# Performance work log

Measured on AMD Instinct MI355X. Metric: run time of the kernel, lower is better.

## Reference

```python
import jax, jax.numpy as jnp
import numpy as np

EMBED = 256
HEADS = 8
LEVELS = 4
POINTS = 4
HD = EMBED // HEADS  # 32


def _bilinear_sample(v, grid):
    """torch.F.grid_sample(mode='bilinear', padding_mode='zeros', align_corners=False).
    v: (B, C, H, W); grid: (B, Q, P, 2) with xy coords in [-1, 1].
    Returns (B, C, Q, P).
    """
    B, C, H, W = v.shape
    x = (grid[..., 0] + 1.0) * (W * 0.5) - 0.5
    y = (grid[..., 1] + 1.0) * (H * 0.5) - 0.5
    x0f = jnp.floor(x)
    y0f = jnp.floor(y)
    wx = x - x0f
    wy = y - y0f
    x0 = x0f.astype(jnp.int32)
    y0 = y0f.astype(jnp.int32)
    vf = v.reshape(B, C, H * W)

    def corner(xi, yi, w):
        valid = (xi >= 0) & (xi < W) & (yi >= 0) & (yi < H)
        idx = jnp.clip(yi, 0, H - 1) * W + jnp.clip(xi, 0, W - 1)  # (B, Q, P)
        g = jax.vmap(lambda vb, ib: jnp.take(vb, ib, axis=1))(vf, idx.reshape(B, -1))
        g = g.reshape(B, C, idx.shape[1], idx.shape[2])  # (B, C, Q, P)
        return g * (w * valid.astype(v.dtype))[:, None]

    return (corner(x0, y0, (1 - wx) * (1 - wy))
            + corner(x0 + 1, y0, wx * (1 - wy))
            + corner(x0, y0 + 1, (1 - wx) * wy)
            + corner(x0 + 1, y0 + 1, wx * wy))


def setup_inputs() -> dict:
    key = jax.random.key(0)
    ks = jax.random.split(key, 16)
    N, Q, D = 2, 8192, EMBED
    inp = {
        'query': jax.random.normal(ks[0], (N, Q, D), jnp.float32),
        'feat0': jax.random.normal(ks[1], (N, D, 64, 64), jnp.float32),
        'feat1': jax.random.normal(ks[2], (N, D, 32, 32), jnp.float32),
        'feat2': jax.random.normal(ks[3], (N, D, 16, 16), jnp.float32),
        'feat3': jax.random.normal(ks[4], (N, D, 8, 8), jnp.float32),
        'reference_points': jax.random.uniform(ks[5], (N, Q, 2), jnp.float32),
        # params stored as (in, out); equivalent math to torch Linear's x @ W.T + b
        'W_off': jax.random.normal(ks[6], (D, HEADS * LEVELS * POINTS * 2), jnp.float32) * 0.01,
        'b_off': jax.random.normal(ks[7], (HEADS * LEVELS * POINTS * 2,), jnp.float32) * 0.01,
        'W_attn': jax.random.normal(ks[8], (D, HEADS * LEVELS * POINTS), jnp.float32) * 0.02,
        'b_attn': jax.random.normal(ks[9], (HEADS * LEVELS * POINTS,), jnp.float32) * 0.02,
        'W_val': jax.random.normal(ks[10], (D, D), jnp.float32) * (1.0 / np.sqrt(D)),
        'b_val': jnp.zeros((D,), jnp.float32),
        'W_out': jax.random.normal(ks[11], (D, D), jnp.float32) * (1.0 / np.sqrt(D)),
        'b_out': jnp.zeros((D,), jnp.float32),
    }
    return inp


def reference(query, feat0, feat1, feat2, feat3, reference_points,
              W_off, b_off, W_attn, b_attn, W_val, b_val, W_out, b_out):
    feats = [feat0, feat1, feat2, feat3]
    N, Q, D = query.shape
    # offset / attention-weight projections
    off = (query @ W_off + b_off).reshape(N, Q, HEADS, LEVELS, POINTS, 2)
    attn = (query @ W_attn + b_attn).reshape(N, Q, HEADS, LEVELS, POINTS)
    # reference points (N,Q,2) -> (N,Q,L,2)
    ref = jnp.broadcast_to(reference_points[:, :, None, :], (N, Q, LEVELS, 2))
    # value projection (1x1 conv) per level, split heads -> (N*H, hd, H_l, W_l)
    vals = [(jnp.einsum('bchw,cd->bdhw', f, W_val) + b_val[None, :, None, None])
            .reshape(N * HEADS, HD, f.shape[2], f.shape[3]) for f in feats]
    # flatten batch*heads
    off = off.transpose(0, 2, 1, 3, 4, 5).reshape(N * HEADS, Q, LEVELS, POINTS, 2)
    attn = attn.transpose(0, 2, 1, 3, 4).reshape(N * HEADS, Q, LEVELS, POINTS)
    refh = jnp.broadcast_to(ref[:, None], (N, HEADS, Q, LEVELS, 2)).reshape(N * HEADS, Q, LEVELS, 2)
    loc = refh[:, :, :, None, :] + off                 # (NH, Q, L, P, 2) in [0,1]
    grid = 2.0 * loc - 1.0                             # [-1, 1]
    # per-level bilinear sampling -> (NH, hd, Q, L, P)
    sampled = jnp.stack([_bilinear_sample(vals[l], grid[:, :, l]) for l in range(LEVELS)], axis=-2)
    # softmax over levels*points
    aw = jax.nn.softmax(attn.reshape(N * HEADS, Q, LEVELS * POINTS), axis=-1)
    aw = jnp.nan_to_num(aw).reshape(N * HEADS, Q, LEVELS, POINTS)
    out = jnp.einsum('bcqlp,bqlp->bcq', sampled, aw)   # (NH, hd, Q)
    out = out.reshape(N, HEADS, HD, Q).transpose(0, 3, 1, 2).reshape(N, Q, D)
    return out @ W_out + b_out
```

## Files before the change

kernel.cpp:

```cpp
#include <hip/hip_runtime.h>
#include <math.h>

#define NB 2
#define QN 8192
#define DIM 256
#define S_TOT 5440

typedef unsigned int uint32;
typedef _Float16 f16;
typedef __attribute__((ext_vector_type(8))) _Float16 h8;
typedef __attribute__((ext_vector_type(2))) _Float16 h2;
typedef __attribute__((ext_vector_type(4))) float f32x4;
typedef __attribute__((ext_vector_type(4))) uint32 u32x4;

__global__ __launch_bounds__(256) void prep_kernel(
    const float* __restrict__ f0, const float* __restrict__ f1,
    const float* __restrict__ f2, const float* __restrict__ f3,
    const float* __restrict__ W_off, const float* __restrict__ W_attn,
    const float* __restrict__ W_val, const float* __restrict__ W_out,
    f16* __restrict__ featT, f16* __restrict__ Wcat_t,
    f16* __restrict__ Wval_t, f16* __restrict__ Wout_t) {
  const int t = blockIdx.x;
  const float* src;
  f16* dst;
  int S, tb;
  if (t < 340) {
    const int b = (t >= 170) ? 1 : 0;
    const int tt = t - 170 * b;
    int soff;
    if (tt < 128)      { src = f0; S = 4096; soff = 0;    tb = tt; }
    else if (tt < 160) { src = f1; S = 1024; soff = 4096; tb = tt - 128; }
    else if (tt < 168) { src = f2; S = 256;  soff = 5120; tb = tt - 160; }
    else               { src = f3; S = 64;   soff = 5376; tb = tt - 168; }
    src += (size_t)b * 256 * S;
    dst = featT + ((size_t)b * S_TOT + soff) * 256;
  } else {
    const int tw = t - 340;
    if (tw < 8)       { src = W_off;  dst = Wcat_t;             S = 256; tb = tw; }
    else if (tw < 12) { src = W_attn; dst = Wcat_t + 256 * 256; S = 128; tb = tw - 8; }
    else if (tw < 20) { src = W_val;  dst = Wval_t;             S = 256; tb = tw - 12; }
    else              { src = W_out;  dst = Wout_t;             S = 256; tb = tw - 20; }
  }
  const int s0 = tb * 32, c0 = blockIdx.y * 32;

  __shared__ float tile[32][33];
  const int tx = threadIdx.x & 31, ty = threadIdx.x >> 5;
#pragma unroll
  for (int j = 0; j < 4; ++j) {
    const int c = c0 + ty + j * 8;
    tile[ty + j * 8][tx] = src[(size_t)c * S + s0 + tx];
  }
  __syncthreads();
#pragma unroll
  for (int j = 0; j < 4; ++j) {
    const int srow = s0 + ty + j * 8;
    dst[(size_t)srow * 256 + c0 + tx] = (f16)tile[tx][ty + j * 8];
  }
}

__global__ __launch_bounds__(256) void gemm_fused_kernel(
    const f16* __restrict__ featT, const float* __restrict__ query,
    const f16* __restrict__ Wval_t, const f16* __restrict__ Wcat_t,
    const float* __restrict__ b_val, const float* __restrict__ b_off,
    const float* __restrict__ b_attn,
    f16* __restrict__ vals, f16* __restrict__ offb, f16* __restrict__ attnb) {
  __shared__ f16 As[64][256];
  __shared__ f16 Bs[64][256];
  const int t = blockIdx.x;
  const int tid = threadIdx.x;
  const bool isval = (t < 170);
  const size_t r0 = (size_t)(isval ? t : t - 170) * 64;
  const int NC = isval ? 4 : 6;
  const f16* Bt = isval ? Wval_t : Wcat_t;

  const int row = tid >> 5, slot = tid & 31;

#pragma unroll
  for (int i = 0; i < 8; ++i) {
    const int r = i * 8 + row;
    const int ph = (slot & 24) | ((slot ^ r) & 7);
    if (isval) {
      *(u32x4*)&As[r][ph * 8] =
          *(const u32x4*)(featT + (r0 + r) * 256 + slot * 8);
    } else {
      const float* ga = query + (r0 + r) * 256 + slot * 8;
      const float4 u0 = *(const float4*)ga;
      const float4 u1 = *(const float4*)(ga + 4);
      h8 hv = {(f16)u0.x, (f16)u0.y, (f16)u0.z, (f16)u0.w,
               (f16)u1.x, (f16)u1.y, (f16)u1.z, (f16)u1.w};
      *(h8*)&As[r][ph * 8] = hv;
    }
  }

  const int wid = tid >> 6, lane = tid & 63;
  const int wr = (wid >> 1) * 32, wc = (wid & 1) * 32;
  const int l15 = lane & 15, l4 = lane >> 4;

  u32x4 bpre[8];
#pragma unroll
  for (int i = 0; i < 8; ++i) {
    bpre[i] = *(const u32x4*)(Bt + (size_t)(i * 8 + row) * 256 + slot * 8);
  }

  h8 areg[8][2];

  for (int c = 0; c < NC; ++c) {
    __syncthreads();
#pragma unroll
    for (int i = 0; i < 8; ++i) {
      const int r = i * 8 + row;
      const int ph = (slot & 24) | ((slot ^ r) & 7);
      *(u32x4*)&Bs[r][ph * 8] = bpre[i];
    }
    __syncthreads();

    if (c + 1 < NC) {
#pragma unroll
      for (int i = 0; i < 8; ++i) {
        bpre[i] = *(const u32x4*)(Bt + (size_t)((c + 1) * 64 + i * 8 + row) * 256 + slot * 8);
      }
    }

    f32x4 acc[2][2] = {};
#pragma unroll
    for (int ks = 0; ks < 8; ++ks) {
      const int slot2 = ks * 4 + l4;
      if (c == 0) {
#pragma unroll
        for (int m = 0; m < 2; ++m) {
          const int r = wr + m * 16 + l15;
          const int ph = (slot2 & 24) | ((slot2 ^ r) & 7);
          areg[ks][m] = *(const h8*)&As[r][ph * 8];
        }
      }
      h8 b[2];
#pragma unroll
      for (int n = 0; n < 2; ++n) {
        const int r = wc + n * 16 + l15;
        const int ph = (slot2 & 24) | ((slot2 ^ r) & 7);
        b[n] = *(const h8*)&Bs[r][ph * 8];
      }
#pragma unroll
      for (int m = 0; m < 2; ++m)
#pragma unroll
        for (int n = 0; n < 2; ++n)
          acc[m][n] = __builtin_amdgcn_mfma_f32_16x16x32_f16(areg[ks][m], b[n], acc[m][n], 0, 0, 0);
    }

#pragma unroll
    for (int m = 0; m < 2; ++m)
#pragma unroll
      for (int n = 0; n < 2; ++n)
#pragma unroll
        for (int r = 0; r < 4; ++r) {
          const size_t rw = r0 + wr + m * 16 + l4 * 4 + r;
          const int col = c * 64 + wc + n * 16 + l15;
          const float v = acc[m][n][r];
          if (isval) {
            vals[rw * 256 + col] = (f16)(v + b_val[col]);
          } else if (col < 256) {
            offb[rw * 256 + col] = (f16)(v + b_off[col]);
          } else {
            attnb[rw * 128 + (col - 256)] = (f16)(v + b_attn[col - 256]);
          }
        }
  }
}

__global__ __launch_bounds__(256) void gemm_out_kernel(
    const f16* __restrict__ A, const f16* __restrict__ Bt,
    const float* __restrict__ bias, float* __restrict__ out) {
  __shared__ f16 As[64][256];
  __shared__ f16 Bs[64][256];
  const int tid = threadIdx.x;
  const size_t r0 = (size_t)blockIdx.x * 64;

  const int row = tid >> 5, slot = tid & 31;
#pragma unroll
  for (int i = 0; i < 8; ++i) {
    const int r = i * 8 + row;
    const int ph = (slot & 24) | ((slot ^ r) & 7);
    *(u32x4*)&As[r][ph * 8] = *(const u32x4*)(A + (r0 + r) * 256 + slot * 8);
  }

  const int wid = tid >> 6, lane = tid & 63;
  const int wr = (wid >> 1) * 32, wc = (wid & 1) * 32;
  const int l15 = lane & 15, l4 = lane >> 4;

  u32x4 bpre[8];
#pragma unroll
  for (int i = 0; i < 8; ++i) {
    bpre[i] = *(const u32x4*)(Bt + (size_t)(i * 8 + row) * 256 + slot * 8);
  }

  h8 areg[8][2];

  for (int c = 0; c < 4; ++c) {
    __syncthreads();
#pragma unroll
    for (int i = 0; i < 8; ++i) {
      const int r = i * 8 + row;
      const int ph = (slot & 24) | ((slot ^ r) & 7);
      *(u32x4*)&Bs[r][ph * 8] = bpre[i];
    }
    __syncthreads();

    if (c + 1 < 4) {
#pragma unroll
      for (int i = 0; i < 8; ++i) {
        bpre[i] = *(const u32x4*)(Bt + (size_t)((c + 1) * 64 + i * 8 + row) * 256 + slot * 8);
      }
    }

    f32x4 acc[2][2] = {};
#pragma unroll
    for (int ks = 0; ks < 8; ++ks) {
      const int slot2 = ks * 4 + l4;
      if (c == 0) {
#pragma unroll
        for (int m = 0; m < 2; ++m) {
          const int r = wr + m * 16 + l15;
          const int ph = (slot2 & 24) | ((slot2 ^ r) & 7);
          areg[ks][m] = *(const h8*)&As[r][ph * 8];
        }
      }
      h8 b[2];
#pragma unroll
      for (int n = 0; n < 2; ++n) {
        const int r = wc + n * 16 + l15;
        const int ph = (slot2 & 24) | ((slot2 ^ r) & 7);
        b[n] = *(const h8*)&Bs[r][ph * 8];
      }
#pragma unroll
      for (int m = 0; m < 2; ++m)
#pragma unroll
        for (int n = 0; n < 2; ++n)
          acc[m][n] = __builtin_amdgcn_mfma_f32_16x16x32_f16(areg[ks][m], b[n], acc[m][n], 0, 0, 0);
    }

#pragma unroll
    for (int m = 0; m < 2; ++m)
#pragma unroll
      for (int n = 0; n < 2; ++n)
#pragma unroll
        for (int r = 0; r < 4; ++r) {
          const size_t rw = r0 + wr + m * 16 + l4 * 4 + r;
          const int col = c * 64 + wc + n * 16 + l15;
          out[rw * 256 + col] = acc[m][n][r] + bias[col];
        }
  }
}

__global__ __launch_bounds__(256) void sample_kernel(
    const f16* __restrict__ vals, const f16* __restrict__ offb,
    const f16* __restrict__ attnb, const float* __restrict__ refp,
    f16* __restrict__ samp) {
  const int tid = threadIdx.x;
  const int g = tid & 15;
  const int grp = tid >> 4;
  const int h = grp & 7;
  const int half = tid >> 7;
  const int bq = blockIdx.x * 2 + half;
  const int b = bq >> 13;

  __shared__ float4 wts[16][17];
  __shared__ int4 idxs[16][17];

  const float rx = refp[(size_t)bq * 2 + 0];
  const float ry = refp[(size_t)bq * 2 + 1];

  float logit = (float)attnb[(size_t)bq * 128 + h * 16 + g];
  float m = logit;
#pragma unroll
  for (int mask = 1; mask < 16; mask <<= 1)
    m = fmaxf(m, __shfl_xor(m, mask, 16));
  const float e = __expf(logit - m);
  float ssum = e;
#pragma unroll
  for (int mask = 1; mask < 16; mask <<= 1)
    ssum += __shfl_xor(ssum, mask, 16);
  const float aw = e / ssum;

  const h2 ov = *(const h2*)(offb + (size_t)bq * 256 + h * 32 + g * 2);
  const int l = g >> 2;
  const int Wl = 64 >> l;
  const int loff = (l == 0) ? 0 : (l == 1) ? 4096 : (l == 2) ? 5120 : 5376;

  const float px = (rx + (float)ov[0]) * (float)Wl - 0.5f;
  const float py = (ry + (float)ov[1]) * (float)Wl - 0.5f;
  const float fx = floorf(px), fy = floorf(py);
  const float wx = px - fx, wy = py - fy;
  const int x0 = (int)fx, y0 = (int)fy;
  const int x1 = x0 + 1, y1 = y0 + 1;
  const float vx0 = (x0 >= 0 && x0 < Wl) ? 1.f : 0.f;
  const float vx1 = (x1 >= 0 && x1 < Wl) ? 1.f : 0.f;
  const float vy0 = (y0 >= 0 && y0 < Wl) ? 1.f : 0.f;
  const float vy1 = (y1 >= 0 && y1 < Wl) ? 1.f : 0.f;
  const int cx0 = min(max(x0, 0), Wl - 1), cx1 = min(max(x1, 0), Wl - 1);
  const int cy0 = min(max(y0, 0), Wl - 1), cy1 = min(max(y1, 0), Wl - 1);
  const int base = b * S_TOT + loff;
  idxs[grp][g] = make_int4((base + cy0 * Wl + cx0) * 512,
                           (base + cy0 * Wl + cx1) * 512,
                           (base + cy1 * Wl + cx0) * 512,
                           (base + cy1 * Wl + cx1) * 512);
  wts[grp][g] = make_float4(aw * (1.f - wx) * (1.f - wy) * vx0 * vy0,
                            aw * wx * (1.f - wy) * vx1 * vy0,
                            aw * (1.f - wx) * wy * vx0 * vy1,
                            aw * wx * wy * vx1 * vy1);
  __syncthreads();

  const int c4 = g & 3, pc = g >> 2;
  const char* vb = (const char*)vals + (h * 64 + c4 * 16);

  float wv[16];
  int ids[16];
#pragma unroll
  for (int pt = 0; pt < 16; ++pt) {
    wv[pt] = ((const float*)&wts[grp][pt])[pc];
    ids[pt] = ((const int*)&idxs[grp][pt])[pc];
  }
  h8 vv[16];
#pragma unroll
  for (int pt = 0; pt < 16; ++pt) vv[pt] = *(const h8*)(vb + ids[pt]);

  float a[8] = {};
#pragma unroll
  for (int pt = 0; pt < 16; ++pt) {
#pragma unroll
    for (int k = 0; k < 8; ++k) a[k] = fmaf((float)vv[pt][k], wv[pt], a[k]);
  }
#pragma unroll
  for (int k = 0; k < 8; ++k) {
    a[k] += __shfl_xor(a[k], 4);
    a[k] += __shfl_xor(a[k], 8);
  }
  if (pc == 0) {
    h8 r;
#pragma unroll
    for (int k = 0; k < 8; ++k) r[k] = (f16)a[k];
    *(h8*)(samp + (size_t)bq * 256 + h * 32 + c4 * 8) = r;
  }
}

extern "C" void kernel_launch(void* const* d_in, const int* in_sizes, int n_in,
                              void* d_out, int out_size, void* d_ws, size_t ws_size,
                              hipStream_t stream) {
  const float* query = (const float*)d_in[0];
  const float* feat[4] = {(const float*)d_in[1], (const float*)d_in[2],
                          (const float*)d_in[3], (const float*)d_in[4]};
  const float* refp  = (const float*)d_in[5];
  const float* W_off = (const float*)d_in[6];
  const float* b_off = (const float*)d_in[7];
  const float* W_attn = (const float*)d_in[8];
  const float* b_attn = (const float*)d_in[9];
  const float* W_val = (const float*)d_in[10];
  const float* b_val = (const float*)d_in[11];
  const float* W_out = (const float*)d_in[12];
  const float* b_out = (const float*)d_in[13];
  float* out = (float*)d_out;

  f16* ws = (f16*)d_ws;
  f16* featT  = ws;
  f16* vals   = featT + (size_t)NB * S_TOT * 256;
  f16* offb   = vals + (size_t)NB * S_TOT * 256;
  f16* samp   = offb + (size_t)NB * QN * 256;
  f16* attnb  = samp + (size_t)NB * QN * 256;
  f16* Wcat_t = attnb + (size_t)NB * QN * 128;
  f16* Wval_t = Wcat_t + 384 * 256;
  f16* Wout_t = Wval_t + 256 * 256;

  prep_kernel<<<dim3(368, 8), 256, 0, stream>>>(
      feat[0], feat[1], feat[2], feat[3], W_off, W_attn, W_val, W_out,
      featT, Wcat_t, Wval_t, Wout_t);

  gemm_fused_kernel<<<170 + 256, 256, 0, stream>>>(
      featT, query, Wval_t, Wcat_t, b_val, b_off, b_attn, vals, offb, attnb);

  sample_kernel<<<(NB * QN) / 2, 256, 0, stream>>>(vals, offb, attnb, refp, samp);

  gemm_out_kernel<<<(NB * QN) / 64, 256, 0, stream>>>(samp, Wout_t, b_out, out);
}
```

Before: 69.28 us.

## Fuse feature transpose into value GEMM and remap sample block order

The feature-map transpose and fp16 conversion move out of the prep kernel and into the value-projection GEMM's A-tile load. Each block now reads fp32 channel-major features directly and scatters them transposed into swizzled shared memory. This removes a full write and re-read of the transposed feature buffer in global memory, at the cost of scalar 2-byte shared-memory stores. The sampling kernel's block-to-query mapping is also changed to interleave the two batches, which may spread value-map accesses across the cache.

```diff
diff --git a/kernel.cpp b/kernel.cpp
--- a/kernel.cpp
+++ b/kernel.cpp
@@ -13,34 +13,16 @@
 typedef __attribute__((ext_vector_type(4))) float f32x4;
 typedef __attribute__((ext_vector_type(4))) uint32 u32x4;
 
-__global__ __launch_bounds__(256) void prep_kernel(
-    const float* __restrict__ f0, const float* __restrict__ f1,
-    const float* __restrict__ f2, const float* __restrict__ f3,
+__global__ __launch_bounds__(256) void prep_w_kernel(
     const float* __restrict__ W_off, const float* __restrict__ W_attn,
     const float* __restrict__ W_val, const float* __restrict__ W_out,
-    f16* __restrict__ featT, f16* __restrict__ Wcat_t,
-    f16* __restrict__ Wval_t, f16* __restrict__ Wout_t) {
+    f16* __restrict__ Wcat_t, f16* __restrict__ Wval_t, f16* __restrict__ Wout_t) {
   const int t = blockIdx.x;
-  const float* src;
-  f16* dst;
-  int S, tb;
-  if (t < 340) {
-    const int b = (t >= 170) ? 1 : 0;
-    const int tt = t - 170 * b;
-    int soff;
-    if (tt < 128)      { src = f0; S = 4096; soff = 0;    tb = tt; }
-    else if (tt < 160) { src = f1; S = 1024; soff = 4096; tb = tt - 128; }
-    else if (tt < 168) { src = f2; S = 256;  soff = 5120; tb = tt - 160; }
-    else               { src = f3; S = 64;   soff = 5376; tb = tt - 168; }
-    src += (size_t)b * 256 * S;
-    dst = featT + ((size_t)b * S_TOT + soff) * 256;
-  } else {
-    const int tw = t - 340;
-    if (tw < 8)       { src = W_off;  dst = Wcat_t;             S = 256; tb = tw; }
-    else if (tw < 12) { src = W_attn; dst = Wcat_t + 256 * 256; S = 128; tb = tw - 8; }
-    else if (tw < 20) { src = W_val;  dst = Wval_t;             S = 256; tb = tw - 12; }
-    else              { src = W_out;  dst = Wout_t;             S = 256; tb = tw - 20; }
-  }
+  const float* src; f16* dst; int S, tb;
+  if (t < 8)       { src = W_off;  dst = Wcat_t;             S = 256; tb = t; }
+  else if (t < 12) { src = W_attn; dst = Wcat_t + 256 * 256; S = 128; tb = t - 8; }
+  else if (t < 20) { src = W_val;  dst = Wval_t;             S = 256; tb = t - 12; }
+  else             { src = W_out;  dst = Wout_t;             S = 256; tb = t - 20; }
   const int s0 = tb * 32, c0 = blockIdx.y * 32;
 
   __shared__ float tile[32][33];
@@ -59,7 +41,9 @@
 }
 
 __global__ __launch_bounds__(256) void gemm_fused_kernel(
-    const f16* __restrict__ featT, const float* __restrict__ query,
+    const float* __restrict__ f0, const float* __restrict__ f1,
+    const float* __restrict__ f2, const float* __restrict__ f3,
+    const float* __restrict__ query,
     const f16* __restrict__ Wval_t, const f16* __restrict__ Wcat_t,
     const float* __restrict__ b_val, const float* __restrict__ b_off,
     const float* __restrict__ b_attn,
@@ -74,15 +58,36 @@
   const f16* Bt = isval ? Wval_t : Wcat_t;
 
   const int row = tid >> 5, slot = tid & 31;
-
-#pragma unroll
-  for (int i = 0; i < 8; ++i) {
-    const int r = i * 8 + row;
-    const int ph = (slot & 24) | ((slot ^ r) & 7);
-    if (isval) {
-      *(u32x4*)&As[r][ph * 8] =
-          *(const u32x4*)(featT + (r0 + r) * 256 + slot * 8);
-    } else {
+  const int lane = tid & 63;
+
+  if (isval) {
+    const int b = (t >= 85) ? 1 : 0;
+    const int tl = t - 85 * b;
+    const float* fsrc; int HW, sl0;
+    if (tl < 64)      { fsrc = f0; HW = 4096; sl0 = tl * 64; }
+    else if (tl < 80) { fsrc = f1; HW = 1024; sl0 = (tl - 64) * 64; }
+    else if (tl < 84) { fsrc = f2; HW = 256;  sl0 = (tl - 80) * 64; }
+    else              { fsrc = f3; HW = 64;   sl0 = 0; }
+    fsrc += (size_t)b * 256 * HW + sl0;
+    const int cw = (tid >> 6) * 64 + (lane >> 4);
+    const int s4 = (lane & 15) * 4;
+#pragma unroll
+    for (int pass = 0; pass < 16; ++pass) {
+      const int c = cw + pass * 4;
+      const float4 v = *(const float4*)(fsrc + (size_t)c * HW + s4);
+      const int sl = c >> 3;
+#pragma unroll
+      for (int j = 0; j < 4; ++j) {
+        const int r = s4 + j;
+        const int ph = (sl & 24) | ((sl ^ r) & 7);
+        As[r][ph * 8 + (c & 7)] = (f16)((const float*)&v)[j];
+      }
+    }
+  } else {
+#pragma unroll
+    for (int i = 0; i < 8; ++i) {
+      const int r = i * 8 + row;
+      const int ph = (slot & 24) | ((slot ^ r) & 7);
       const float* ga = query + (r0 + r) * 256 + slot * 8;
       const float4 u0 = *(const float4*)ga;
       const float4 u1 = *(const float4*)(ga + 4);
@@ -92,7 +97,7 @@
     }
   }
 
-  const int wid = tid >> 6, lane = tid & 63;
+  const int wid = tid >> 6;
   const int wr = (wid >> 1) * 32, wc = (wid & 1) * 32;
   const int l15 = lane & 15, l4 = lane >> 4;
 
@@ -260,8 +265,10 @@
   const int grp = tid >> 4;
   const int h = grp & 7;
   const int half = tid >> 7;
-  const int bq = blockIdx.x * 2 + half;
-  const int b = bq >> 13;
+  const int bi = blockIdx.x;
+  const int b = (bi >> 2) & 1;
+  const int wb = (bi >> 3) * 4 + (bi & 3);
+  const int bq = b * QN + wb * 2 + half;
 
   __shared__ float4 wts[16][17];
   __shared__ int4 idxs[16][17];
@@ -360,8 +367,7 @@
   float* out = (float*)d_out;
 
   f16* ws = (f16*)d_ws;
-  f16* featT  = ws;
-  f16* vals   = featT + (size_t)NB * S_TOT * 256;
+  f16* vals   = ws;
   f16* offb   = vals + (size_t)NB * S_TOT * 256;
   f16* samp   = offb + (size_t)NB * QN * 256;
   f16* attnb  = samp + (size_t)NB * QN * 256;
@@ -369,12 +375,12 @@
   f16* Wval_t = Wcat_t + 384 * 256;
   f16* Wout_t = Wval_t + 256 * 256;
 
-  prep_kernel<<<dim3(368, 8), 256, 0, stream>>>(
-      feat[0], feat[1], feat[2], feat[3], W_off, W_attn, W_val, W_out,
-      featT, Wcat_t, Wval_t, Wout_t);
+  prep_w_kernel<<<dim3(28, 8), 256, 0, stream>>>(
+      W_off, W_attn, W_val, W_out, Wcat_t, Wval_t, Wout_t);
 
   gemm_fused_kernel<<<170 + 256, 256, 0, stream>>>(
-      featT, query, Wval_t, Wcat_t, b_val, b_off, b_attn, vals, offb, attnb);
+      feat[0], feat[1], feat[2], feat[3], query, Wval_t, Wcat_t,
+      b_val, b_off, b_attn, vals, offb, attnb);
 
   sample_kernel<<<(NB * QN) / 2, 256, 0, stream>>>(vals, offb, attnb, refp, samp);
 
```

Result: no change. 69.78 us (+0.7%).
